# Optimization experiments

Hardware: AMD Instinct MI355X
Metric: run time of the kernel (lower is better)

## Reference

```python
import jax, jax.numpy as jnp
import numpy as np
from jax import lax

NIMG = 4          # num_image_channels (dx for these is zeroed each step)
C = 64            # total channels = 4 + 44 + 16
NFILT = 2         # learned depthwise filters
HID = 256         # hidden_size
FIRE = 0.5        # fire_rate
B, H, W = 16, 128, 128
STEPS = 8


def setup_inputs() -> dict:
    key = jax.random.key(0)
    ks = jax.random.split(key, 7)
    x = jax.random.normal(ks[0], (B, H, W, C), jnp.float32)
    # depthwise 3x3 kernels, OIHW with I=1 (groups = C)
    w_conv1 = jax.random.normal(ks[1], (C, 1, 3, 3), jnp.float32) * 0.3
    w_conv2 = jax.random.normal(ks[2], (C, 1, 3, 3), jnp.float32) * 0.3
    fan_in = C * (NFILT + 1)  # 192
    w_hidden = jax.random.normal(ks[3], (HID, fan_in), jnp.float32) / np.sqrt(fan_in).astype(np.float32)
    b_hidden = jax.random.normal(ks[4], (HID,), jnp.float32) * 0.01
    # original zero-inits final_layer; use small random weights for a nontrivial baseline
    w_final = jax.random.normal(ks[5], (C, HID), jnp.float32) * 0.02
    rand_vals = jax.random.uniform(ks[6], (STEPS, B, H, W, 1), jnp.float32)
    return {"x": x, "w_conv1": w_conv1, "w_conv2": w_conv2,
            "w_hidden": w_hidden, "b_hidden": b_hidden, "w_final": w_final,
            "rand_vals": rand_vals, "steps": STEPS}


def _dwconv(xc, w):
    # xc: [B, C, W, H]; reflect-pad then valid depthwise 3x3 (groups=C)
    xp = jnp.pad(xc, ((0, 0), (0, 0), (1, 1), (1, 1)), mode='reflect')
    return lax.conv_general_dilated(xp, w, (1, 1), 'VALID',
                                    dimension_numbers=('NCHW', 'OIHW', 'NCHW'),
                                    feature_group_count=C)


def reference(x, w_conv1, w_conv2, w_hidden, b_hidden, w_final, rand_vals, steps):
    dtype = x.dtype
    ch_mask = (jnp.arange(C) >= NIMG).astype(dtype)  # zero image-channel updates

    def step(xc, rnd):
        # xc: [B, C, W, H]  (torch layout after x.transpose(1,3))
        y = jnp.concatenate([xc, _dwconv(xc, w_conv1), _dwconv(xc, w_conv2)], axis=1)  # [B,3C,W,H]
        yt = jnp.transpose(y, (0, 3, 2, 1))  # [B,H,W,3C]
        h = jax.nn.relu(jnp.einsum('bhwf,of->bhwo', yt, w_hidden) + b_hidden)
        dx = jnp.einsum('bhwo,co->bhwc', h, w_final)  # [B,H,W,C]
        dx = dx * (rnd > FIRE).astype(dtype) * ch_mask  # stochastic gate + immutable image channels
        xc = xc + jnp.transpose(dx, (0, 3, 2, 1))
        life = (xc[:, 0:1] > 0).astype(dtype)  # channel-0 life mask broadcast over channels
        return xc * life, None

    xc0 = jnp.transpose(x, (0, 3, 2, 1))  # NHWC -> [B,C,W,H]
    xcN, _ = lax.scan(step, xc0, rand_vals)
    return jnp.transpose(xcN, (0, 3, 2, 1))  # back to NHWC
```

## Files before the change

### kernel.cpp

```cpp
#include <hip/hip_runtime.h>

#define BB 16
#define HH 128
#define WW 128
#define CH 64
#define TPX 32
#define NTH 256
#define NPIX (BB*HH*WW)
#define KF 192
#define HID 256

#define WS_WTP 0u
#define WS_WFP 98304u
#define WS_WCB 131072u
#define WS_ST  135680u

typedef __attribute__((ext_vector_type(8))) short short8;
typedef __attribute__((ext_vector_type(8))) unsigned short ushort8;
typedef __attribute__((ext_vector_type(4))) float f4;
typedef __attribute__((ext_vector_type(2))) float f2;
typedef __attribute__((ext_vector_type(4))) unsigned int u32x4;

#define OFF_FC  13056
#define OFF_STG 16384
#define OFF_WCV 21248
#define OFF_LG  25856
#define SMEM_SZ 26112

#define GLDS16(gp, lp) __builtin_amdgcn_global_load_lds( \
    (const __attribute__((address_space(1))) unsigned int*)(gp), \
    (__attribute__((address_space(3))) unsigned int*)(lp), 16, 0, 0)

__device__ __forceinline__ unsigned short f2b(float f) {
    unsigned x = __float_as_uint(f);
    x += 0x7fffu + ((x >> 16) & 1u);
    return (unsigned short)(x >> 16);
}
__device__ __forceinline__ unsigned cvtpk(float a, float b) {
    unsigned r;
    asm("v_cvt_pk_bf16_f32 %0, %1, %2" : "=v"(r) : "v"(a), "v"(b));
    return r;
}
__device__ __forceinline__ float b2f(unsigned short u) {
    return __uint_as_float(((unsigned)u) << 16);
}
__device__ __forceinline__ int refl(int i, int n) {
    if (i < 0) return -i;
    if (i >= n) return 2*n - 2 - i;
    return i;
}
__device__ __forceinline__ int xrow(int row, int chunk) {
    return row*64 + (((chunk ^ row) & 7) << 3);
}

__global__ __launch_bounds__(256) void prep(
    const float* __restrict__ wh, const float* __restrict__ wf,
    unsigned short* __restrict__ wtp, unsigned short* __restrict__ wfp)
{
    int i = blockIdx.x * 256 + threadIdx.x;
    if (i < 6144) {
        const int l = i & 63, r = i >> 6;
        const int ks = r % 6, ti = r / 6;
        const int row = ti*16 + (l & 15);
        const int k0  = ks*32 + (l >> 4)*8;
        ushort8 v;
        #pragma unroll
        for (int j = 0; j < 8; ++j) v[j] = f2b(wh[row*KF + k0 + j]);
        *(ushort8*)&wtp[(size_t)i * 8] = v;
    } else {
        const int g = i - 6144;
        const int l = g & 63, r = g >> 6;
        const int ks2 = r & 7, cq = r >> 3;
        const int c  = cq*16 + (l & 15);
        const int o0 = ks2*32 + (l >> 4)*8;
        ushort8 v;
        #pragma unroll
        for (int j = 0; j < 8; ++j) v[j] = f2b(wf[c*HID + o0 + j]);
        *(ushort8*)&wfp[(size_t)g * 8] = v;
    }
}

__global__ __launch_bounds__(256) void prep2(
    const float* __restrict__ w1, const float* __restrict__ w2,
    float* __restrict__ wcb)
{
    int i = blockIdx.x * 256 + threadIdx.x;
    if (i < 1152) {
        const int f = i / 576, rem = i - f * 576;
        const int t = rem >> 6, c = rem & 63;
        wcb[i] = (f ? w2 : w1)[c*9 + t];
    }
}

template<int SRCF, int DSTF>
__global__ __launch_bounds__(256, 4) void nca_step(
    const float* __restrict__ xinf, const unsigned short* __restrict__ srcb,
    void* __restrict__ dstv,
    const unsigned short* __restrict__ wtp, const unsigned short* __restrict__ wfp,
    const float* __restrict__ wcbg,
    const float* __restrict__ bh, const float* __restrict__ rnd)
{
    __shared__ __align__(16) char smem[SMEM_SZ];
    unsigned short* xs   = (unsigned short*)smem;
    char*           fch  = smem + OFF_FC;
    char*           stg  = smem + OFF_STG;
    float*          wcvb = (float*)(smem + OFF_WCV);
    float*          lgs  = (float*)(smem + OFF_LG);

    const int tid = threadIdx.x;
    const int l = tid & 63, wv = tid >> 6;
    const int lr = l & 15, gq = l >> 4;
    const int w0 = blockIdx.x * TPX;
    const int h  = blockIdx.y;
    const int b  = blockIdx.z;
    const int R  = b * HH + h;

    if (SRCF == 1) {
        #pragma unroll
        for (int it = 0; it < 3; ++it) {
            const int g = wv + it*4;
            const int c = g*64 + l;
            const int row = c >> 3, ckp = c & 7;
            const int r3 = row / 34, px = row - r3*34;
            const int ck = ckp ^ (row & 7);
            const int sr = refl(h - 1 + r3, HH);
            const int sc = refl(w0 - 1 + px, WW);
            const unsigned short* gp = srcb + ((((size_t)b*HH + sr)*WW + sc) << 6) + (ck << 3);
            GLDS16(gp, (char*)xs + (size_t)g*1024);
        }
        if (wv == 0 && l < 48) {
            const int c = 768 + l;
            const int row = c >> 3, ckp = c & 7;
            const int r3 = row / 34, px = row - r3*34;
            const int ck = ckp ^ (row & 7);
            const int sr = refl(h - 1 + r3, HH);
            const int sc = refl(w0 - 1 + px, WW);
            const unsigned short* gp = srcb + ((((size_t)b*HH + sr)*WW + sc) << 6) + (ck << 3);
            GLDS16(gp, (char*)xs + (size_t)12*1024);
        }
    } else {
        const int q = tid & 3;
        for (int s0 = tid >> 2; s0 < 102; s0 += 64) {
            const int r3 = s0 / 34, wi = s0 - r3*34;
            const int sr = refl(h - 1 + r3, HH);
            const int sc = refl(w0 - 1 + wi, WW);
            const size_t pix = ((size_t)b*HH + sr)*WW + sc;
            const float* p = xinf + pix*64 + q*16;
            f4 a0 = *(const f4*)p, a1 = *(const f4*)(p+4);
            f4 a2 = *(const f4*)(p+8), a3 = *(const f4*)(p+12);
            u32x4 o0, o1;
            o0[0] = cvtpk(a0.x, a0.y); o0[1] = cvtpk(a0.z, a0.w);
            o0[2] = cvtpk(a1.x, a1.y); o0[3] = cvtpk(a1.z, a1.w);
            o1[0] = cvtpk(a2.x, a2.y); o1[1] = cvtpk(a2.z, a2.w);
            o1[2] = cvtpk(a3.x, a3.y); o1[3] = cvtpk(a3.z, a3.w);
            const int row = r3*34 + wi;
            *(u32x4*)(xs + xrow(row, 2*q))     = o0;
            *(u32x4*)(xs + xrow(row, 2*q + 1)) = o1;
        }
    }
    for (int j = tid; j < 288; j += NTH)
        ((f4*)wcvb)[j] = ((const f4*)wcbg)[j];
    if (tid < TPX) {
        const size_t pix = (size_t)R * WW + w0 + tid;
        lgs[TPX + tid] = (rnd[pix] > 0.5f) ? 1.f : 0.f;
        if (SRCF == 0)
            lgs[tid] = (xinf[pix*64] > 0.f) ? 1.f : 0.f;
    }
    __syncthreads();

    if (SRCF == 1 && tid < TPX)
        lgs[tid] = (b2f(xs[xrow(34 + tid + 1, 0)]) > 0.f) ? 1.f : 0.f;

    {
        const int px = tid >> 3, ck = tid & 7, cg = ck * 8;
        f2 a1[4], a2[4];
        #pragma unroll
        for (int k2 = 0; k2 < 4; ++k2) { a1[k2] = (f2){0.f,0.f}; a2[k2] = (f2){0.f,0.f}; }
        #pragma unroll
        for (int t = 0; t < 9; ++t) {
            const int i2 = t / 3, j = t - 3*i2;
            const u32x4 xv = *(const u32x4*)(xs + xrow(j*34 + px + i2, ck));
            const f2* w1p = (const f2*)(wcvb + t*64 + cg);
            const f2* w2p = (const f2*)(wcvb + 576 + t*64 + cg);
            #pragma unroll
            for (int k2 = 0; k2 < 4; ++k2) {
                const unsigned d = xv[k2];
                f2 xf;
                xf.x = __uint_as_float(d << 16);
                xf.y = __uint_as_float(d & 0xffff0000u);
                a1[k2] = __builtin_elementwise_fma(xf, w1p[k2], a1[k2]);
                a2[k2] = __builtin_elementwise_fma(xf, w2p[k2], a2[k2]);
            }
        }
        u32x4 o1v, o2v;
        #pragma unroll
        for (int k2 = 0; k2 < 4; ++k2) {
            o1v[k2] = cvtpk(a1[k2].x, a1[k2].y);
            o2v[k2] = cvtpk(a2[k2].x, a2[k2].y);
        }
        const int sw = (px & 7) << 4;
        *(u32x4*)(fch + ((px*256 + cg*2) ^ sw))       = o1v;
        *(u32x4*)(fch + ((px*256 + 128 + cg*2) ^ sw)) = o2v;
    }
    __syncthreads();

    f4 acc[2][4];
    #pragma unroll
    for (int ot = 0; ot < 4; ++ot) {
        const float bv = bh[wv*64 + ot*16 + lr];
        const f4 bvv = {bv, bv, bv, bv};
        acc[0][ot] = bvv; acc[1][ot] = bvv;
    }
    #pragma unroll
    for (int ks = 0; ks < 6; ++ks) {
        short8 afr[2];
        #pragma unroll
        for (int mt = 0; mt < 2; ++mt) {
            const int px = mt*16 + lr;
            if (ks < 2)
                afr[mt] = *(const short8*)(xs + xrow(34 + px + 1, ks*4 + gq));
            else
                afr[mt] = *(const short8*)(fch +
                            ((px*256 + (ks-2)*64 + gq*16) ^ ((px & 7) << 4)));
        }
        #pragma unroll
        for (int ot = 0; ot < 4; ++ot) {
            const short8 bfr = *(const short8*)(wtp + ((((wv*4 + ot)*6 + ks)*64 + l) << 3));
            acc[0][ot] = __builtin_amdgcn_mfma_f32_16x16x32_bf16(afr[0], bfr, acc[0][ot], 0,0,0);
            acc[1][ot] = __builtin_amdgcn_mfma_f32_16x16x32_bf16(afr[1], bfr, acc[1][ot], 0,0,0);
        }
    }

    const int mh = wv >> 1, cs = wv & 1;
    unsigned short baseb[8];
    #pragma unroll
    for (int ct = 0; ct < 2; ++ct)
      #pragma unroll
      for (int r2 = 0; r2 < 4; ++r2) {
        const int px = mh*16 + gq*4 + r2;
        const int c  = cs*32 + ct*16 + lr;
        baseb[ct*4 + r2] = xs[xrow(34 + px + 1, c >> 3) + (c & 7)];
      }
    __syncthreads();

    #pragma unroll
    for (int mt = 0; mt < 2; ++mt)
      #pragma unroll
      for (int ot = 0; ot < 4; ++ot) {
        const unsigned p01 = cvtpk(fmaxf(acc[mt][ot][0], 0.f), fmaxf(acc[mt][ot][1], 0.f));
        const unsigned p23 = cvtpk(fmaxf(acc[mt][ot][2], 0.f), fmaxf(acc[mt][ot][3], 0.f));
        const int o = wv*64 + ot*16 + lr;
        const int px0 = mt*16 + gq*4;
        *(unsigned short*)(smem + (((px0+0)*512 + o*2) ^ (((px0+0) & 7) << 4))) = (unsigned short)p01;
        *(unsigned short*)(smem + (((px0+1)*512 + o*2) ^ (((px0+1) & 7) << 4))) = (unsigned short)(p01 >> 16);
        *(unsigned short*)(smem + (((px0+2)*512 + o*2) ^ (((px0+2) & 7) << 4))) = (unsigned short)p23;
        *(unsigned short*)(smem + (((px0+3)*512 + o*2) ^ (((px0+3) & 7) << 4))) = (unsigned short)(p23 >> 16);
      }
    __syncthreads();

    f4 acc2[2] = {{0.f,0.f,0.f,0.f},{0.f,0.f,0.f,0.f}};
    #pragma unroll
    for (int ks2 = 0; ks2 < 8; ++ks2) {
        const int px = mh*16 + lr;
        const short8 ha = *(const short8*)(smem + ((px*512 + ks2*64 + gq*16) ^ ((px & 7) << 4)));
        #pragma unroll
        for (int ct = 0; ct < 2; ++ct) {
            const short8 bw = *(const short8*)(wfp + ((((cs*2 + ct)*8 + ks2)*64 + l) << 3));
            acc2[ct] = __builtin_amdgcn_mfma_f32_16x16x32_bf16(ha, bw, acc2[ct], 0,0,0);
        }
    }

    unsigned short* stageB = (unsigned short*)stg;
    float*          stageF = (float*)stg;
    #pragma unroll
    for (int r2 = 0; r2 < 4; ++r2) {
        const int px = mh*16 + gq*4 + r2;
        const float life = lgs[px], g = lgs[TPX + px];
        float outv[2];
        #pragma unroll
        for (int ct = 0; ct < 2; ++ct) {
            const int c  = cs*32 + ct*16 + lr;
            const float base = b2f(baseb[ct*4 + r2]);
            const float dx   = acc2[ct][r2];
            outv[ct] = (c >= 4) ? (base + dx * g) * life : base * life;
        }
        const int c0 = cs*32 + lr;
        if (DSTF == 1) {
            stageF[px*64 + c0]      = outv[0];
            stageF[px*64 + c0 + 16] = outv[1];
        } else {
            const unsigned p = cvtpk(outv[0], outv[1]);
            stageB[px*64 + c0]      = (unsigned short)p;
            stageB[px*64 + c0 + 16] = (unsigned short)(p >> 16);
        }
    }
    __syncthreads();

    const size_t pix0 = (size_t)R * WW + w0;
    if (DSTF == 1) {
        float* dstf = (float*)dstv + pix0 * 64;
        for (int i = tid; i < 512; i += NTH) {
            const f4 v = *(const f4*)(stageF + i*4);
            __builtin_nontemporal_store(v, (f4*)(dstf + i*4));
        }
    } else {
        unsigned short* dstb = (unsigned short*)dstv + pix0 * 64;
        const ushort8 v = *(const ushort8*)(stageB + tid*8);
        __builtin_nontemporal_store(v, (ushort8*)(dstb + tid*8));
    }
}

extern "C" void kernel_launch(void* const* d_in, const int* in_sizes, int n_in,
                              void* d_out, int out_size, void* d_ws, size_t ws_size,
                              hipStream_t stream) {
    const float* xin = (const float*)d_in[0];
    const float* w1  = (const float*)d_in[1];
    const float* w2  = (const float*)d_in[2];
    const float* wh  = (const float*)d_in[3];
    const float* bh  = (const float*)d_in[4];
    const float* wf  = (const float*)d_in[5];
    const float* rv  = (const float*)d_in[6];

    unsigned short* wtp = (unsigned short*)((char*)d_ws + WS_WTP);
    unsigned short* wfp = (unsigned short*)((char*)d_ws + WS_WFP);
    float*          wcb = (float*)((char*)d_ws + WS_WCB);
    unsigned short* stb = (unsigned short*)((char*)d_ws + WS_ST);
    unsigned short* omb = (unsigned short*)d_out;

    prep <<<dim3(32), dim3(256), 0, stream>>>(wh, wf, wtp, wfp);
    prep2<<<dim3(5),  dim3(256), 0, stream>>>(w1, w2, wcb);

    dim3 g(WW / TPX, HH, BB), blk(NTH);
    nca_step<0,0><<<g, blk, 0, stream>>>(xin, nullptr, stb, wtp, wfp, wcb, bh, rv);
    for (int s = 1; s < 7; ++s) {
        const unsigned short* sp = (s & 1) ? stb : omb;
        unsigned short* dp       = (s & 1) ? omb : stb;
        nca_step<1,0><<<g, blk, 0, stream>>>(nullptr, sp, dp, wtp, wfp, wcb, bh,
                                             rv + (size_t)s * NPIX);
    }
    nca_step<1,1><<<g, blk, 0, stream>>>(nullptr, stb, d_out, wtp, wfp, wcb, bh,
                                         rv + (size_t)7 * NPIX);
}
```

Baseline: 581.2 us.

## Process two rows per block with 512 threads and reuse halo rows

```diff
diff --git a/kernel.cpp b/kernel.cpp
--- a/kernel.cpp
+++ b/kernel.cpp
@@ -5,7 +5,9 @@
 #define WW 128
 #define CH 64
 #define TPX 32
-#define NTH 256
+#define NROW 2
+#define NPX  64
+#define NTH 512
 #define NPIX (BB*HH*WW)
 #define KF 192
 #define HID 256
@@ -21,11 +23,10 @@
 typedef __attribute__((ext_vector_type(2))) float f2;
 typedef __attribute__((ext_vector_type(4))) unsigned int u32x4;
 
-#define OFF_FC  13056
-#define OFF_STG 16384
-#define OFF_WCV 21248
-#define OFF_LG  25856
-#define SMEM_SZ 26112
+#define OFF_FC  17408
+#define OFF_LG  33792
+#define SMEM_SZ 34304
+
 
 #define GLDS16(gp, lp) __builtin_amdgcn_global_load_lds( \
     (const __attribute__((address_space(1))) unsigned int*)(gp), \
@@ -93,56 +94,53 @@
 }
 
 template<int SRCF, int DSTF>
-__global__ __launch_bounds__(256, 4) void nca_step(
+__global__ __launch_bounds__(512, 4) void nca_step(
     const float* __restrict__ xinf, const unsigned short* __restrict__ srcb,
     void* __restrict__ dstv,
     const unsigned short* __restrict__ wtp, const unsigned short* __restrict__ wfp,
-    const float* __restrict__ wcbg,
+    const float* __restrict__ wcvb,
     const float* __restrict__ bh, const float* __restrict__ rnd)
 {
     __shared__ __align__(16) char smem[SMEM_SZ];
-    unsigned short* xs   = (unsigned short*)smem;
-    char*           fch  = smem + OFF_FC;
-    char*           stg  = smem + OFF_STG;
-    float*          wcvb = (float*)(smem + OFF_WCV);
-    float*          lgs  = (float*)(smem + OFF_LG);
+    unsigned short* xs  = (unsigned short*)smem;
+    char*           fch = smem + OFF_FC;
+    float*          lgs = (float*)(smem + OFF_LG);
 
     const int tid = threadIdx.x;
     const int l = tid & 63, wv = tid >> 6;
     const int lr = l & 15, gq = l >> 4;
     const int w0 = blockIdx.x * TPX;
-    const int h  = blockIdx.y;
+    const int h0 = blockIdx.y * NROW;
     const int b  = blockIdx.z;
-    const int R  = b * HH + h;
 
     if (SRCF == 1) {
         #pragma unroll
-        for (int it = 0; it < 3; ++it) {
-            const int g = wv + it*4;
+        for (int it = 0; it < 2; ++it) {
+            const int g = wv + it*8;
             const int c = g*64 + l;
             const int row = c >> 3, ckp = c & 7;
             const int r3 = row / 34, px = row - r3*34;
             const int ck = ckp ^ (row & 7);
-            const int sr = refl(h - 1 + r3, HH);
+            const int sr = refl(h0 - 1 + r3, HH);
             const int sc = refl(w0 - 1 + px, WW);
             const unsigned short* gp = srcb + ((((size_t)b*HH + sr)*WW + sc) << 6) + (ck << 3);
             GLDS16(gp, (char*)xs + (size_t)g*1024);
         }
-        if (wv == 0 && l < 48) {
-            const int c = 768 + l;
+        if (wv == 0) {
+            const int c = 1024 + l;
             const int row = c >> 3, ckp = c & 7;
             const int r3 = row / 34, px = row - r3*34;
             const int ck = ckp ^ (row & 7);
-            const int sr = refl(h - 1 + r3, HH);
+            const int sr = refl(h0 - 1 + r3, HH);
             const int sc = refl(w0 - 1 + px, WW);
             const unsigned short* gp = srcb + ((((size_t)b*HH + sr)*WW + sc) << 6) + (ck << 3);
-            GLDS16(gp, (char*)xs + (size_t)12*1024);
+            GLDS16(gp, (char*)xs + (size_t)16*1024);
         }
     } else {
         const int q = tid & 3;
-        for (int s0 = tid >> 2; s0 < 102; s0 += 64) {
+        for (int s0 = tid >> 2; s0 < 136; s0 += 128) {
             const int r3 = s0 / 34, wi = s0 - r3*34;
-            const int sr = refl(h - 1 + r3, HH);
+            const int sr = refl(h0 - 1 + r3, HH);
             const int sc = refl(w0 - 1 + wi, WW);
             const size_t pix = ((size_t)b*HH + sr)*WW + sc;
             const float* p = xinf + pix*64 + q*16;
@@ -153,33 +151,31 @@
             o0[2] = cvtpk(a1.x, a1.y); o0[3] = cvtpk(a1.z, a1.w);
             o1[0] = cvtpk(a2.x, a2.y); o1[1] = cvtpk(a2.z, a2.w);
             o1[2] = cvtpk(a3.x, a3.y); o1[3] = cvtpk(a3.z, a3.w);
-            const int row = r3*34 + wi;
-            *(u32x4*)(xs + xrow(row, 2*q))     = o0;
-            *(u32x4*)(xs + xrow(row, 2*q + 1)) = o1;
-        }
-    }
-    for (int j = tid; j < 288; j += NTH)
-        ((f4*)wcvb)[j] = ((const f4*)wcbg)[j];
-    if (tid < TPX) {
-        const size_t pix = (size_t)R * WW + w0 + tid;
-        lgs[TPX + tid] = (rnd[pix] > 0.5f) ? 1.f : 0.f;
+            *(u32x4*)(xs + xrow(s0, 2*q))     = o0;
+            *(u32x4*)(xs + xrow(s0, 2*q + 1)) = o1;
+        }
+    }
+    if (tid < NPX) {
+        const size_t pix = ((size_t)b*HH + h0 + (tid >> 5))*WW + w0 + (tid & 31);
+        lgs[NPX + tid] = (rnd[pix] > 0.5f) ? 1.f : 0.f;
         if (SRCF == 0)
             lgs[tid] = (xinf[pix*64] > 0.f) ? 1.f : 0.f;
     }
     __syncthreads();
 
-    if (SRCF == 1 && tid < TPX)
-        lgs[tid] = (b2f(xs[xrow(34 + tid + 1, 0)]) > 0.f) ? 1.f : 0.f;
+    if (SRCF == 1 && tid < NPX)
+        lgs[tid] = (b2f(xs[xrow(((tid >> 5) + 1)*34 + (tid & 31) + 1, 0)]) > 0.f) ? 1.f : 0.f;
 
     {
         const int px = tid >> 3, ck = tid & 7, cg = ck * 8;
+        const int rbase = px >> 5, col = px & 31;
         f2 a1[4], a2[4];
         #pragma unroll
         for (int k2 = 0; k2 < 4; ++k2) { a1[k2] = (f2){0.f,0.f}; a2[k2] = (f2){0.f,0.f}; }
         #pragma unroll
         for (int t = 0; t < 9; ++t) {
             const int i2 = t / 3, j = t - 3*i2;
-            const u32x4 xv = *(const u32x4*)(xs + xrow(j*34 + px + i2, ck));
+            const u32x4 xv = *(const u32x4*)(xs + xrow((rbase + j)*34 + col + i2, ck));
             const f2* w1p = (const f2*)(wcvb + t*64 + cg);
             const f2* w2p = (const f2*)(wcvb + 576 + t*64 + cg);
             #pragma unroll
@@ -204,30 +200,32 @@
     }
     __syncthreads();
 
-    f4 acc[2][4];
-    #pragma unroll
-    for (int ot = 0; ot < 4; ++ot) {
-        const float bv = bh[wv*64 + ot*16 + lr];
+    f4 acc[4][2];
+    #pragma unroll
+    for (int ot = 0; ot < 2; ++ot) {
+        const float bv = bh[wv*32 + ot*16 + lr];
         const f4 bvv = {bv, bv, bv, bv};
-        acc[0][ot] = bvv; acc[1][ot] = bvv;
+        #pragma unroll
+        for (int mt = 0; mt < 4; ++mt) acc[mt][ot] = bvv;
     }
     #pragma unroll
     for (int ks = 0; ks < 6; ++ks) {
-        short8 afr[2];
-        #pragma unroll
-        for (int mt = 0; mt < 2; ++mt) {
+        short8 afr[4];
+        #pragma unroll
+        for (int mt = 0; mt < 4; ++mt) {
             const int px = mt*16 + lr;
             if (ks < 2)
-                afr[mt] = *(const short8*)(xs + xrow(34 + px + 1, ks*4 + gq));
+                afr[mt] = *(const short8*)(xs + xrow(((px >> 5) + 1)*34 + (px & 31) + 1, ks*4 + gq));
             else
                 afr[mt] = *(const short8*)(fch +
                             ((px*256 + (ks-2)*64 + gq*16) ^ ((px & 7) << 4)));
         }
         #pragma unroll
-        for (int ot = 0; ot < 4; ++ot) {
-            const short8 bfr = *(const short8*)(wtp + ((((wv*4 + ot)*6 + ks)*64 + l) << 3));
-            acc[0][ot] = __builtin_amdgcn_mfma_f32_16x16x32_bf16(afr[0], bfr, acc[0][ot], 0,0,0);
-            acc[1][ot] = __builtin_amdgcn_mfma_f32_16x16x32_bf16(afr[1], bfr, acc[1][ot], 0,0,0);
+        for (int ot = 0; ot < 2; ++ot) {
+            const short8 bfr = *(const short8*)(wtp + ((((wv*2 + ot)*6 + ks)*64 + l) << 3));
+            #pragma unroll
+            for (int mt = 0; mt < 4; ++mt)
+                acc[mt][ot] = __builtin_amdgcn_mfma_f32_16x16x32_bf16(afr[mt], bfr, acc[mt][ot], 0,0,0);
         }
     }
 
@@ -239,17 +237,17 @@
       for (int r2 = 0; r2 < 4; ++r2) {
         const int px = mh*16 + gq*4 + r2;
         const int c  = cs*32 + ct*16 + lr;
-        baseb[ct*4 + r2] = xs[xrow(34 + px + 1, c >> 3) + (c & 7)];
+        baseb[ct*4 + r2] = xs[xrow(((px >> 5) + 1)*34 + (px & 31) + 1, c >> 3) + (c & 7)];
       }
     __syncthreads();
 
     #pragma unroll
-    for (int mt = 0; mt < 2; ++mt)
+    for (int mt = 0; mt < 4; ++mt)
       #pragma unroll
-      for (int ot = 0; ot < 4; ++ot) {
+      for (int ot = 0; ot < 2; ++ot) {
         const unsigned p01 = cvtpk(fmaxf(acc[mt][ot][0], 0.f), fmaxf(acc[mt][ot][1], 0.f));
         const unsigned p23 = cvtpk(fmaxf(acc[mt][ot][2], 0.f), fmaxf(acc[mt][ot][3], 0.f));
-        const int o = wv*64 + ot*16 + lr;
+        const int o = wv*32 + ot*16 + lr;
         const int px0 = mt*16 + gq*4;
         *(unsigned short*)(smem + (((px0+0)*512 + o*2) ^ (((px0+0) & 7) << 4))) = (unsigned short)p01;
         *(unsigned short*)(smem + (((px0+1)*512 + o*2) ^ (((px0+1) & 7) << 4))) = (unsigned short)(p01 >> 16);
@@ -269,13 +267,14 @@
             acc2[ct] = __builtin_amdgcn_mfma_f32_16x16x32_bf16(ha, bw, acc2[ct], 0,0,0);
         }
     }
-
-    unsigned short* stageB = (unsigned short*)stg;
-    float*          stageF = (float*)stg;
+    __syncthreads();
+
+    unsigned short* stageB = (unsigned short*)smem;
+    float*          stageF = (float*)smem;
     #pragma unroll
     for (int r2 = 0; r2 < 4; ++r2) {
         const int px = mh*16 + gq*4 + r2;
-        const float life = lgs[px], g = lgs[TPX + px];
+        const float life = lgs[px], g = lgs[NPX + px];
         float outv[2];
         #pragma unroll
         for (int ct = 0; ct < 2; ++ct) {
@@ -296,17 +295,22 @@
     }
     __syncthreads();
 
-    const size_t pix0 = (size_t)R * WW + w0;
     if (DSTF == 1) {
-        float* dstf = (float*)dstv + pix0 * 64;
-        for (int i = tid; i < 512; i += NTH) {
-            const f4 v = *(const f4*)(stageF + i*4);
-            __builtin_nontemporal_store(v, (f4*)(dstf + i*4));
+        float* dstf = (float*)dstv;
+        #pragma unroll
+        for (int it = 0; it < 2; ++it) {
+            const int i = tid + it*512;
+            const int px = i >> 4, c4 = (i & 15) * 4;
+            const size_t pix = ((size_t)b*HH + h0 + (px >> 5))*WW + w0 + (px & 31);
+            const f4 v = *(const f4*)(stageF + px*64 + c4);
+            __builtin_nontemporal_store(v, (f4*)(dstf + pix*64 + c4));
         }
     } else {
-        unsigned short* dstb = (unsigned short*)dstv + pix0 * 64;
-        const ushort8 v = *(const ushort8*)(stageB + tid*8);
-        __builtin_nontemporal_store(v, (ushort8*)(dstb + tid*8));
+        unsigned short* dstb = (unsigned short*)dstv;
+        const int px = tid >> 3, c8 = (tid & 7) * 8;
+        const size_t pix = ((size_t)b*HH + h0 + (px >> 5))*WW + w0 + (px & 31);
+        const ushort8 v = *(const ushort8*)(stageB + px*64 + c8);
+        __builtin_nontemporal_store(v, (ushort8*)(dstb + pix*64 + c8));
     }
 }
 
@@ -330,7 +334,7 @@
     prep <<<dim3(32), dim3(256), 0, stream>>>(wh, wf, wtp, wfp);
     prep2<<<dim3(5),  dim3(256), 0, stream>>>(w1, w2, wcb);
 
-    dim3 g(WW / TPX, HH, BB), blk(NTH);
+    dim3 g(WW / TPX, HH / NROW, BB), blk(NTH);
     nca_step<0,0><<<g, blk, 0, stream>>>(xin, nullptr, stb, wtp, wfp, wcb, bh, rv);
     for (int s = 1; s < 7; ++s) {
         const unsigned short* sp = (s & 1) ? stb : omb;
```

Measured after the change: 704.0 us. 21.1% more time.
